# Performance work log

Measured on AMD Instinct MI355X. Metric: run time of the kernel, lower is better.

## Reference

```python
import jax, jax.numpy as jnp
import numpy as np

D_MODEL = 1024
NHEAD = 16
HEAD_DIM = D_MODEL // NHEAD
SF_THRESHOLD = 4.0
SF_LEVELS = 8
STEP = SF_THRESHOLD / SF_LEVELS  # quantization step of ScaleAndFireNeuron
EPS = 1e-6


def setup_inputs() -> dict:
    key = jax.random.key(0)
    ks = jax.random.split(key, 12)
    B, L, D = 2, 2048, D_MODEL
    s = 1.0 / np.sqrt(D)
    inp = {
        "x": jax.random.normal(ks[0], (B, L, D), dtype=jnp.float32),
        "wq": jax.random.normal(ks[1], (D, D), dtype=jnp.float32) * s,
        "bq": jnp.zeros((D,), dtype=jnp.float32),
        "wk": jax.random.normal(ks[2], (D, D), dtype=jnp.float32) * s,
        "bk": jnp.zeros((D,), dtype=jnp.float32),
        "wv": jax.random.normal(ks[3], (D, D), dtype=jnp.float32) * s,
        "bv": jnp.zeros((D,), dtype=jnp.float32),
        "wo": jax.random.normal(ks[4], (D, D), dtype=jnp.float32) * s,
        "bo": jnp.zeros((D,), dtype=jnp.float32),
        "gq": jnp.ones((HEAD_DIM,), dtype=jnp.float32),  # SpikingQKNorm gain (q)
        "gk": jnp.ones((HEAD_DIM,), dtype=jnp.float32),  # SpikingQKNorm gain (k)
    }
    return inp


def _rms_norm(t, g):
    # SpikingQKNorm: RMS normalization over head_dim with learned gain
    return t * jax.lax.rsqrt(jnp.mean(t * t, axis=-1, keepdims=True) + EPS) * g


def _sfn(t):
    # ScaleAndFireNeuron: T=1 multi-level spike quantization with straight-through estimator.
    # Levels are integer multiples of STEP, clipped to +/- SF_LEVELS.
    q = jnp.clip(jnp.round(t / STEP), -SF_LEVELS, SF_LEVELS) * STEP
    return t + jax.lax.stop_gradient(q - t)


def reference(x, wq, bq, wk, bk, wv, bv, wo, bo, gq, gk):
    B, L, D = x.shape
    H, Dh = NHEAD, HEAD_DIM
    scale = Dh ** -0.5

    def proj(w, b):
        return (x @ w.T + b).reshape(B, L, H, Dh).transpose(0, 2, 1, 3)  # [B,H,L,Dh]

    q = _sfn(_rms_norm(proj(wq, bq), gq))
    k = _sfn(_rms_norm(proj(wk, bk), gk))
    v = _sfn(proj(wv, bv))

    scores = jnp.einsum('bhqd,bhkd->bhqk', q, k) * scale  # [B,H,L,L]
    probs = jax.nn.softmax(scores, axis=-1)
    out = jnp.einsum('bhqk,bhkd->bhqd', probs, v)  # [B,H,L,Dh]
    out = out.transpose(0, 2, 1, 3).reshape(B, L, D)
    return out @ wo.T + bo
```

## Files before the change

kernel.cpp:

```cpp
#include <hip/hip_runtime.h>
#include <stdint.h>

#define D_MODEL 1024
#define NHEAD 16
#define HEAD_DIM 64
#define SEQ 2048
#define BATCH 2
#define MROWS (BATCH*SEQ)
#define KVBLK 128
#define KVTILES (SEQ/KVBLK)

typedef unsigned short u16;
typedef short bf16x8 __attribute__((ext_vector_type(8)));
typedef float f32x4 __attribute__((ext_vector_type(4)));
typedef float f32x16 __attribute__((ext_vector_type(16)));

__device__ inline float bf2f(u16 h){ return __uint_as_float(((unsigned)h)<<16); }
__device__ inline u16 f2bf(float x){
  unsigned u = __float_as_uint(x);
  unsigned r = (u + 0x7FFFu + ((u>>16)&1u)) >> 16;
  return (u16)r;
}

__device__ inline f32x4 mfma_bf16(bf16x8 a, bf16x8 b, f32x4 c){
  return __builtin_amdgcn_mfma_f32_16x16x32_bf16(a, b, c, 0, 0, 0);
}
__device__ inline f32x16 mfma32_bf16(bf16x8 a, bf16x8 b, f32x16 c){
  return __builtin_amdgcn_mfma_f32_32x32x16_bf16(a, b, c, 0, 0, 0);
}

__device__ inline void gld_lds16(const u16* g, u16* l){
  __builtin_amdgcn_global_load_lds(
      (const __attribute__((address_space(1))) void*)g,
      (__attribute__((address_space(3))) void*)l, 16, 0, 0);
}

__device__ inline int swz8(int row){ return (row ^ (row >> 3)) & 7; }

__device__ inline uint32_t pack_bf2(float p0, float p1){
  uint32_t u0 = __float_as_uint(p0) + 0x8000u;
  uint32_t u1 = __float_as_uint(p1) + 0x8000u;
  return __builtin_amdgcn_perm(u1, u0, 0x07060302u);
}

__global__ __launch_bounds__(256) void pack_all(
    const float* __restrict__ x,
    const float* __restrict__ wq, const float* __restrict__ wk,
    const float* __restrict__ wv, const float* __restrict__ wo,
    u16* __restrict__ x_hi, u16* __restrict__ x_lo,
    u16* __restrict__ qkv_hi, u16* __restrict__ qkv_lo,
    u16* __restrict__ wo_hi)
{
  int b = blockIdx.x;
  const float* src;
  u16 *hi, *lo;
  int i;
  if (b < 4096){
    src = x; i = b*256 + threadIdx.x;
    hi = x_hi; lo = x_lo;
  } else {
    int which = (b - 4096) >> 10;
    i = ((b - 4096) & 1023)*256 + threadIdx.x;
    src = which==0 ? wq : which==1 ? wk : which==2 ? wv : wo;
    if (which == 3){ hi = wo_hi; lo = nullptr; }
    else { hi = qkv_hi + ((size_t)which << 20); lo = qkv_lo + ((size_t)which << 20); }
  }
  float4 v = ((const float4*)src)[i];
  float vv[4] = {v.x, v.y, v.z, v.w};
  u16 h[4], l[4];
  #pragma unroll
  for (int j=0;j<4;j++){
    h[j] = f2bf(vv[j]);
    l[j] = f2bf(vv[j] - bf2f(h[j]));
  }
  ((ushort4*)hi)[i] = make_ushort4(h[0],h[1],h[2],h[3]);
  if (lo) ((ushort4*)lo)[i] = make_ushort4(l[0],l[1],l[2],l[3]);
}

__global__ __launch_bounds__(256) void gemm_qkv(
    const u16* __restrict__ a_hi, const u16* __restrict__ a_lo,
    const u16* __restrict__ b_hi, const u16* __restrict__ b_lo,
    const float* __restrict__ bq, const float* __restrict__ bk_,
    const float* __restrict__ bv,
    u16* __restrict__ qb, u16* __restrict__ kb, u16* __restrict__ vb,
    const float* __restrict__ gq, const float* __restrict__ gk)
{
  __shared__ u16 lds[2][12288];
  const int tid = threadIdx.x;
  const int lane = tid & 63;
  const int w = tid >> 6;
  const int wr = w >> 1, wc = w & 1;
  const int m0 = blockIdx.x * 128;
  const int n0 = blockIdx.y * 128;
  const int K = 1024;

  f32x4 acc[4][4];
  #pragma unroll
  for (int i=0;i<4;i++)
    #pragma unroll
    for (int j=0;j<4;j++) acc[i][j] = (f32x4){0.f,0.f,0.f,0.f};

  auto stage = [&](int buf, int kt){
    u16* base = &lds[buf][0];
    if (kt < 32){
      int kk = kt << 5;
      #pragma unroll
      for (int r=0;r<2;r++){
        const u16* g = a_hi + (size_t)(m0 + (tid>>2) + r*64)*K + kk + (tid&3)*8;
        gld_lds16(g, base + w*512 + r*2048);
      }
      #pragma unroll
      for (int r=0;r<2;r++){
        const u16* g = a_lo + (size_t)(m0 + (tid>>2) + r*64)*K + kk + (tid&3)*8;
        gld_lds16(g, base + 4096 + w*512 + r*2048);
      }
      #pragma unroll
      for (int r=0;r<2;r++){
        const u16* g = b_hi + (size_t)(n0 + (tid>>2) + r*64)*K + kk + (tid&3)*8;
        gld_lds16(g, base + 8192 + w*512 + r*2048);
      }
    } else {
      int kk = (kt-32) << 5;
      #pragma unroll
      for (int r=0;r<2;r++){
        const u16* g = a_hi + (size_t)(m0 + (tid>>2) + r*64)*K + kk + (tid&3)*8;
        gld_lds16(g, base + w*512 + r*2048);
      }
      #pragma unroll
      for (int r=0;r<2;r++){
        const u16* g = b_lo + (size_t)(n0 + (tid>>2) + r*64)*K + kk + (tid&3)*8;
        gld_lds16(g, base + 8192 + w*512 + r*2048);
      }
    }
  };

  const int koff = (lane>>4)*8;
  const int rowa = wr*64 + (lane&15);
  const int rowb = wc*64 + (lane&15);

  stage(0, 0);
  for (int kt=0; kt<64; ++kt){
    __syncthreads();
    if (kt+1 < 64) stage((kt+1)&1, kt+1);
    const u16* la = &lds[kt&1][0];
    const u16* lb = &lds[kt&1][8192];
    bf16x8 bfv[4];
    #pragma unroll
    for (int j=0;j<4;j++) bfv[j] = *(const bf16x8*)&lb[(rowb + j*16)*32 + koff];
    bf16x8 af[4];
    #pragma unroll
    for (int i=0;i<4;i++) af[i] = *(const bf16x8*)&la[(rowa + i*16)*32 + koff];
    #pragma unroll
    for (int i=0;i<4;i++)
      #pragma unroll
      for (int j=0;j<4;j++)
        acc[i][j] = mfma_bf16(af[i], bfv[j], acc[i][j]);
    if (kt < 32){
      const u16* ll = &lds[kt&1][4096];
      bf16x8 al[4];
      #pragma unroll
      for (int i=0;i<4;i++) al[i] = *(const bf16x8*)&ll[(rowa + i*16)*32 + koff];
      #pragma unroll
      for (int i=0;i<4;i++)
        #pragma unroll
        for (int j=0;j<4;j++)
          acc[i][j] = mfma_bf16(al[i], bfv[j], acc[i][j]);
    }
  }

  const int gcolbase = n0 + wc*64;
  const int sidx = gcolbase >> 6;
  const int ttype = sidx < 16 ? 0 : (sidx < 32 ? 1 : 2);
  u16* dst = ttype==0 ? qb : (ttype==1 ? kb : vb);
  const float* bsrc = ttype==0 ? bq : (ttype==1 ? bk_ : bv);
  const int h = sidx - (ttype==1 ? 16 : (ttype==2 ? 32 : 0));
  float gvals[4], bvals[4];
  #pragma unroll
  for (int j=0;j<4;j++){
    int dh = j*16 + (lane&15);
    bvals[j] = bsrc[((gcolbase & 1023) + dh) & 1023];
    gvals[j] = ttype==0 ? gq[dh] : (ttype==1 ? gk[dh] : 1.0f);
  }
  #pragma unroll
  for (int i=0;i<4;i++){
    #pragma unroll
    for (int r=0;r<4;r++){
      float tv[4];
      float ssq = 0.f;
      #pragma unroll
      for (int j=0;j<4;j++){ tv[j] = acc[i][j][r] + bvals[j]; ssq += tv[j]*tv[j]; }
      ssq += __shfl_xor(ssq, 1);
      ssq += __shfl_xor(ssq, 2);
      ssq += __shfl_xor(ssq, 4);
      ssq += __shfl_xor(ssq, 8);
      float s = 1.0f;
      if (ttype < 2) s = 1.0f / sqrtf(ssq * (1.0f/64.0f) + 1e-6f);
      int row = m0 + wr*64 + i*16 + (lane>>4)*4 + r;
      int bi = row >> 11, li = row & 2047;
      size_t obase = ((size_t)(bi*NHEAD + h)*SEQ + li)*HEAD_DIM;
      #pragma unroll
      for (int j=0;j<4;j++){
        float val = tv[j] * s * gvals[j];
        float z = rintf(val * 2.0f);
        z = fminf(8.0f, fmaxf(-8.0f, z));
        dst[obase + j*16 + (lane&15)] = f2bf(z * 0.5f);
      }
    }
  }
}

__global__ __launch_bounds__(256) void gemm_bt(
    const u16* __restrict__ a_hi, const u16* __restrict__ b_hi,
    const float* __restrict__ bias, float* __restrict__ out_f,
    int M, int N, int K)
{
  __shared__ u16 lds[2][8192];
  const int tid = threadIdx.x;
  const int lane = tid & 63;
  const int w = tid >> 6;
  const int wr = w >> 1, wc = w & 1;
  const int m0 = blockIdx.x * 128;
  const int n0 = blockIdx.y * 128;
  const int NT = K / 32;

  f32x4 acc[4][4];
  #pragma unroll
  for (int i=0;i<4;i++)
    #pragma unroll
    for (int j=0;j<4;j++) acc[i][j] = (f32x4){0.f,0.f,0.f,0.f};

  auto stage = [&](int buf, int kt){
    int kk = kt * 32;
    u16* base = &lds[buf][0];
    #pragma unroll
    for (int r=0;r<2;r++){
      const u16* g = a_hi + (size_t)(m0 + (tid>>2) + r*64)*K + kk + (tid&3)*8;
      gld_lds16(g, base + w*512 + r*2048);
    }
    #pragma unroll
    for (int r=0;r<2;r++){
      const u16* g = b_hi + (size_t)(n0 + (tid>>2) + r*64)*K + kk + (tid&3)*8;
      gld_lds16(g, base + 4096 + w*512 + r*2048);
    }
  };

  stage(0, 0);
  for (int kt=0; kt<NT; ++kt){
    __syncthreads();
    if (kt+1 < NT) stage((kt+1)&1, kt+1);
    const u16* la = &lds[kt&1][0];
    const u16* lb = &lds[kt&1][4096];
    const int koff = (lane>>4)*8;
    const int rowa = wr*64 + (lane&15);
    const int rowb = wc*64 + (lane&15);
    bf16x8 af[4], bfv[4];
    #pragma unroll
    for (int i=0;i<4;i++) af[i]  = *(const bf16x8*)&la[(rowa + i*16)*32 + koff];
    #pragma unroll
    for (int i=0;i<4;i++) bfv[i] = *(const bf16x8*)&lb[(rowb + i*16)*32 + koff];
    #pragma unroll
    for (int i=0;i<4;i++)
      #pragma unroll
      for (int j=0;j<4;j++)
        acc[i][j] = mfma_bf16(af[i], bfv[j], acc[i][j]);
  }

  const int gcolbase = n0 + wc*64;
  #pragma unroll
  for (int j=0;j<4;j++){
    float bj = bias[gcolbase + j*16 + (lane&15)];
    #pragma unroll
    for (int i=0;i<4;i++){
      int row = m0 + wr*64 + i*16 + (lane>>4)*4;
      #pragma unroll
      for (int r=0;r<4;r++)
        out_f[(size_t)(row+r)*N + gcolbase + j*16 + (lane&15)] = acc[i][j][r] + bj;
    }
  }
}

__global__ __launch_bounds__(256) void transpose_v(const u16* __restrict__ v, u16* __restrict__ vt){
  __shared__ u16 tl[64][66];
  int bh = blockIdx.x >> 5;
  int l0 = (blockIdx.x & 31) * 64;
  int tid = threadIdx.x;
  #pragma unroll
  for (int it=0; it<2; ++it){
    int idx = tid + it*256;
    int row = idx >> 3, g = idx & 7;
    bf16x8 d = *(const bf16x8*)(v + ((size_t)bh*SEQ + l0 + row)*64 + g*8);
    #pragma unroll
    for (int j=0;j<8;j++) tl[row][g*8+j] = (u16)d[j];
  }
  __syncthreads();
  #pragma unroll
  for (int it=0; it<2; ++it){
    int idx = tid + it*256;
    int dh = idx >> 3, g = idx & 7;
    u16 tmp[8];
    #pragma unroll
    for (int j=0;j<8;j++) tmp[j] = tl[g*8+j][dh];
    *(bf16x8*)(vt + ((size_t)bh*HEAD_DIM + dh)*SEQ + l0 + g*8) = *(const bf16x8*)tmp;
  }
}

__global__ __launch_bounds__(256) void attn_kernel(
    const u16* __restrict__ qb, const u16* __restrict__ kb, const u16* __restrict__ vt,
    u16* __restrict__ attn_out)
{
  __shared__ u16 lds_k[2][KVBLK*64];
  __shared__ u16 lds_v[2][64*KVBLK];
  const int tid = threadIdx.x, lane = tid & 63, w = tid >> 6;
  const int bh = blockIdx.y;
  const int q0 = blockIdx.x * 128;
  const size_t kvbase = (size_t)bh * SEQ * HEAD_DIM;
  const size_t vtbase = (size_t)bh * HEAD_DIM * SEQ;
  const int l31 = lane & 31, hi = lane >> 5;

  bf16x8 qf[4];
  #pragma unroll
  for (int kd=0; kd<4; kd++){
    const u16* g = qb + kvbase + (size_t)(q0 + w*32 + l31)*64 + kd*16 + hi*8;
    bf16x8 v = *(const bf16x8*)g;
    #pragma unroll
    for (int j=0;j<8;j++) ((u16*)&v)[j] = f2bf(bf2f((u16)v[j]) * 0.125f);
    qf[kd] = v;
  }

  float l_s = 0.f;
  f32x16 o0, o1;
  #pragma unroll
  for (int r=0;r<16;r++){ o0[r] = 0.f; o1[r] = 0.f; }

  auto stage = [&](int buf, int t){
    const int kv0 = t * KVBLK;
    #pragma unroll
    for (int r=0;r<4;r++){
      int idx = tid + r*256;
      int row = idx >> 3, grp = idx & 7;
      const u16* g = kb + kvbase + (size_t)(kv0 + row)*64 + ((grp ^ swz8(row))<<3);
      gld_lds16(g, &lds_k[buf][idx<<3]);
    }
    #pragma unroll
    for (int r=0;r<4;r++){
      int idx = tid + r*256;
      int row = idx >> 4, grp = idx & 15;
      const u16* g = vt + vtbase + (size_t)row*SEQ + kv0 + ((grp ^ swz8(row))<<3);
      gld_lds16(g, &lds_v[buf][idx<<3]);
    }
  };

  stage(0, 0);
  for (int t=0; t<KVTILES; ++t){
    __syncthreads();
    if (t+1 < KVTILES) stage((t+1)&1, t+1);
    const int buf = t & 1;

    #pragma unroll
    for (int half=0; half<2; ++half){
      f32x16 s0, s1;
      #pragma unroll
      for (int r=0;r<16;r++){ s0[r] = 0.f; s1[r] = 0.f; }
      const int row0 = half*64 + l31;
      const int row1 = half*64 + 32 + l31;
      __builtin_amdgcn_s_setprio(1);
      #pragma unroll
      for (int kd=0; kd<4; kd++){
        bf16x8 a0 = *(const bf16x8*)&lds_k[buf][row0*64 + (((kd*2+hi) ^ swz8(row0))<<3)];
        bf16x8 a1 = *(const bf16x8*)&lds_k[buf][row1*64 + (((kd*2+hi) ^ swz8(row1))<<3)];
        s0 = mfma32_bf16(a0, qf[kd], s0);
        s1 = mfma32_bf16(a1, qf[kd], s1);
      }
      __builtin_amdgcn_s_setprio(0);

      float rsum = 0.f;
      #pragma unroll
      for (int r=0;r<16;r++){ float p = __expf(s0[r]); s0[r] = p; rsum += p; }
      #pragma unroll
      for (int r=0;r<16;r++){ float p = __expf(s1[r]); s1[r] = p; rsum += p; }
      rsum += __shfl_xor(rsum, 32);
      l_s += rsum;

      uint32_t W[2][4][2];
      #pragma unroll
      for (int g=0; g<4; g++){
        W[0][g][0] = pack_bf2(s0[g*4+0], s0[g*4+1]);
        W[0][g][1] = pack_bf2(s0[g*4+2], s0[g*4+3]);
        W[1][g][0] = pack_bf2(s1[g*4+0], s1[g*4+1]);
        W[1][g][1] = pack_bf2(s1[g*4+2], s1[g*4+3]);
      }
      bf16x8 pa[4];
      #pragma unroll
      for (int ks=0; ks<4; ks++){
        const int kvb = ks >> 1, ks0 = ks & 1;
        uint32_t own0 = hi ? W[kvb][ks0*2+1][0] : W[kvb][ks0*2][0];
        uint32_t own1 = hi ? W[kvb][ks0*2+1][1] : W[kvb][ks0*2][1];
        uint32_t t0   = hi ? W[kvb][ks0*2][0]   : W[kvb][ks0*2+1][0];
        uint32_t t1   = hi ? W[kvb][ks0*2][1]   : W[kvb][ks0*2+1][1];
        uint32_t sw0  = (uint32_t)__shfl_xor((int)t0, 32);
        uint32_t sw1  = (uint32_t)__shfl_xor((int)t1, 32);
        uint32_t words[4];
        words[0] = hi ? sw0 : own0;
        words[1] = hi ? sw1 : own1;
        words[2] = hi ? own0 : sw0;
        words[3] = hi ? own1 : sw1;
        pa[ks] = *(const bf16x8*)words;
      }

      __builtin_amdgcn_s_setprio(1);
      #pragma unroll
      for (int ks=0; ks<4; ks++){
        const int rv0 = l31, rv1 = 32 + l31;
        const int cg = half*8 + ks*2 + hi;
        bf16x8 vb0 = *(const bf16x8*)&lds_v[buf][rv0*KVBLK + ((cg ^ swz8(rv0))<<3)];
        bf16x8 vb1 = *(const bf16x8*)&lds_v[buf][rv1*KVBLK + ((cg ^ swz8(rv1))<<3)];
        o0 = mfma32_bf16(pa[ks], vb0, o0);
        o1 = mfma32_bf16(pa[ks], vb1, o1);
      }
      __builtin_amdgcn_s_setprio(0);
    }
  }

  const int b = bh >> 4, h = bh & 15;
  #pragma unroll
  for (int r=0;r<16;r++){
    int q = (r&3) + 8*(r>>2) + 4*hi;
    float linv = 1.0f / __shfl(l_s, q);
    int row = q0 + w*32 + q;
    size_t obase = ((size_t)b*SEQ + row)*D_MODEL + h*64;
    attn_out[obase + l31]      = f2bf(o0[r] * linv);
    attn_out[obase + 32 + l31] = f2bf(o1[r] * linv);
  }
}

extern "C" void kernel_launch(void* const* d_in, const int* in_sizes, int n_in,
                              void* d_out, int out_size, void* d_ws, size_t ws_size,
                              hipStream_t stream){
  const float* x  = (const float*)d_in[0];
  const float* wq = (const float*)d_in[1];
  const float* bq = (const float*)d_in[2];
  const float* wk = (const float*)d_in[3];
  const float* bk = (const float*)d_in[4];
  const float* wv = (const float*)d_in[5];
  const float* bv = (const float*)d_in[6];
  const float* wo = (const float*)d_in[7];
  const float* bo = (const float*)d_in[8];
  const float* gq = (const float*)d_in[9];
  const float* gk = (const float*)d_in[10];
  float* out = (float*)d_out;

  char* ws = (char*)d_ws;
  size_t off = 0;
  auto alloc = [&](size_t bytes) -> char* {
    char* p = ws + off; off += (bytes + 255) & ~(size_t)255; return p;
  };
  const size_t ND = (size_t)MROWS * D_MODEL;
  u16* x_hi    = (u16*)alloc(ND*2);
  u16* x_lo    = (u16*)alloc(ND*2);
  u16* wqkv_hi = (u16*)alloc((size_t)3072*1024*2);
  u16* wqkv_lo = (u16*)alloc((size_t)3072*1024*2);
  u16* wo_hi   = (u16*)alloc((size_t)1024*1024*2);
  u16* q_bf    = (u16*)alloc(ND*2);
  u16* k_bf    = (u16*)alloc(ND*2);
  u16* v_bf    = (u16*)alloc(ND*2);
  u16* vT      = (u16*)alloc(ND*2);
  u16* attn_bf = (u16*)alloc(ND*2);
  (void)ws_size; (void)in_sizes; (void)n_in; (void)out_size;

  pack_all<<<8192, 256, 0, stream>>>(x, wq, wk, wv, wo,
        x_hi, x_lo, wqkv_hi, wqkv_lo, wo_hi);

  gemm_qkv<<<dim3(32,24), 256, 0, stream>>>(x_hi, x_lo, wqkv_hi, wqkv_lo,
        bq, bk, bv, q_bf, k_bf, v_bf, gq, gk);

  transpose_v<<<1024, 256, 0, stream>>>(v_bf, vT);

  attn_kernel<<<dim3(16,32), 256, 0, stream>>>(q_bf, k_bf, vT, attn_bf);

  gemm_bt<<<dim3(32,8), 256, 0, stream>>>(attn_bf, wo_hi, bo, out, MROWS, 1024, 1024);
}
```

Baseline: 172.8 us.

## Switch GEMMs to fp16 split precision and write V transposed from QKV epilogue

Moves the hi/lo split packing and the projection GEMMs from bf16 to fp16 MFMA, and stores the attention output in fp16. This gives more mantissa bits per term and may allow a cheaper split later. Separately, the QKV GEMM epilogue now writes V directly in transposed layout with ushort4 stores, which removes the transpose_v kernel launch and its round trip through memory. fp16 can overflow if activations grow large, and the transposed stores are strided along SEQ, so they may coalesce less well.

New measurement: 170.9 us. About the same (-1.1%).

```diff
diff --git a/kernel.cpp b/kernel.cpp
--- a/kernel.cpp
+++ b/kernel.cpp
@@ -12,6 +12,7 @@
 
 typedef unsigned short u16;
 typedef short bf16x8 __attribute__((ext_vector_type(8)));
+typedef _Float16 f16x8 __attribute__((ext_vector_type(8)));
 typedef float f32x4 __attribute__((ext_vector_type(4)));
 typedef float f32x16 __attribute__((ext_vector_type(16)));
 
@@ -21,9 +22,11 @@
   unsigned r = (u + 0x7FFFu + ((u>>16)&1u)) >> 16;
   return (u16)r;
 }
-
-__device__ inline f32x4 mfma_bf16(bf16x8 a, bf16x8 b, f32x4 c){
-  return __builtin_amdgcn_mfma_f32_16x16x32_bf16(a, b, c, 0, 0, 0);
+__device__ inline u16 f2h(float x){ _Float16 h = (_Float16)x; return *(u16*)&h; }
+__device__ inline float h2f(u16 b){ _Float16 h = *(_Float16*)&b; return (float)h; }
+
+__device__ inline f32x4 mfma_f16(f16x8 a, f16x8 b, f32x4 c){
+  return __builtin_amdgcn_mfma_f32_16x16x32_f16(a, b, c, 0, 0, 0);
 }
 __device__ inline f32x16 mfma32_bf16(bf16x8 a, bf16x8 b, f32x16 c){
   return __builtin_amdgcn_mfma_f32_32x32x16_bf16(a, b, c, 0, 0, 0);
@@ -48,41 +51,49 @@
     const float* __restrict__ wq, const float* __restrict__ wk,
     const float* __restrict__ wv, const float* __restrict__ wo,
     u16* __restrict__ x_hi, u16* __restrict__ x_lo,
-    u16* __restrict__ qkv_hi, u16* __restrict__ qkv_lo,
-    u16* __restrict__ wo_hi)
+    u16* __restrict__ qkv_h, u16* __restrict__ qkv_lo,
+    u16* __restrict__ wo_h)
 {
   int b = blockIdx.x;
-  const float* src;
-  u16 *hi, *lo;
-  int i;
   if (b < 4096){
-    src = x; i = b*256 + threadIdx.x;
-    hi = x_hi; lo = x_lo;
+    int i = b*256 + threadIdx.x;
+    float4 v = ((const float4*)x)[i];
+    float vv[4] = {v.x, v.y, v.z, v.w};
+    u16 h[4], l[4];
+    #pragma unroll
+    for (int j=0;j<4;j++){
+      h[j] = f2h(vv[j]);
+      l[j] = f2h(vv[j] - h2f(h[j]));
+    }
+    ((ushort4*)x_hi)[i] = make_ushort4(h[0],h[1],h[2],h[3]);
+    ((ushort4*)x_lo)[i] = make_ushort4(l[0],l[1],l[2],l[3]);
   } else {
     int which = (b - 4096) >> 10;
-    i = ((b - 4096) & 1023)*256 + threadIdx.x;
-    src = which==0 ? wq : which==1 ? wk : which==2 ? wv : wo;
-    if (which == 3){ hi = wo_hi; lo = nullptr; }
-    else { hi = qkv_hi + ((size_t)which << 20); lo = qkv_lo + ((size_t)which << 20); }
-  }
-  float4 v = ((const float4*)src)[i];
-  float vv[4] = {v.x, v.y, v.z, v.w};
-  u16 h[4], l[4];
-  #pragma unroll
-  for (int j=0;j<4;j++){
-    h[j] = f2bf(vv[j]);
-    l[j] = f2bf(vv[j] - bf2f(h[j]));
-  }
-  ((ushort4*)hi)[i] = make_ushort4(h[0],h[1],h[2],h[3]);
-  if (lo) ((ushort4*)lo)[i] = make_ushort4(l[0],l[1],l[2],l[3]);
+    int i = ((b - 4096) & 1023)*256 + threadIdx.x;
+    const float* src = which==0 ? wq : which==1 ? wk : which==2 ? wv : wo;
+    float4 v = ((const float4*)src)[i];
+    float vv[4] = {v.x, v.y, v.z, v.w};
+    u16 h[4];
+    #pragma unroll
+    for (int j=0;j<4;j++) h[j] = f2h(vv[j]);
+    if (which == 3){
+      ((ushort4*)wo_h)[i] = make_ushort4(h[0],h[1],h[2],h[3]);
+    } else {
+      u16 l[4];
+      #pragma unroll
+      for (int j=0;j<4;j++) l[j] = f2h(vv[j] - h2f(h[j]));
+      ((ushort4*)(qkv_h  + ((size_t)which << 20)))[i] = make_ushort4(h[0],h[1],h[2],h[3]);
+      ((ushort4*)(qkv_lo + ((size_t)which << 20)))[i] = make_ushort4(l[0],l[1],l[2],l[3]);
+    }
+  }
 }
 
 __global__ __launch_bounds__(256) void gemm_qkv(
     const u16* __restrict__ a_hi, const u16* __restrict__ a_lo,
-    const u16* __restrict__ b_hi, const u16* __restrict__ b_lo,
+    const u16* __restrict__ b_h,  const u16* __restrict__ b_lo,
     const float* __restrict__ bq, const float* __restrict__ bk_,
     const float* __restrict__ bv,
-    u16* __restrict__ qb, u16* __restrict__ kb, u16* __restrict__ vb,
+    u16* __restrict__ qb, u16* __restrict__ kb, u16* __restrict__ vt,
     const float* __restrict__ gq, const float* __restrict__ gk)
 {
   __shared__ u16 lds[2][12288];
@@ -90,6 +101,7 @@
   const int lane = tid & 63;
   const int w = tid >> 6;
   const int wr = w >> 1, wc = w & 1;
+  const int l15 = lane & 15, lq = lane >> 4;
   const int m0 = blockIdx.x * 128;
   const int n0 = blockIdx.y * 128;
   const int K = 1024;
@@ -116,7 +128,7 @@
       }
       #pragma unroll
       for (int r=0;r<2;r++){
-        const u16* g = b_hi + (size_t)(n0 + (tid>>2) + r*64)*K + kk + (tid&3)*8;
+        const u16* g = b_h + (size_t)(n0 + (tid>>2) + r*64)*K + kk + (tid&3)*8;
         gld_lds16(g, base + 8192 + w*512 + r*2048);
       }
     } else {
@@ -134,9 +146,9 @@
     }
   };
 
-  const int koff = (lane>>4)*8;
-  const int rowa = wr*64 + (lane&15);
-  const int rowb = wc*64 + (lane&15);
+  const int koff = lq*8;
+  const int rowa = wr*64 + l15;
+  const int rowb = wc*64 + l15;
 
   stage(0, 0);
   for (int kt=0; kt<64; ++kt){
@@ -144,73 +156,99 @@
     if (kt+1 < 64) stage((kt+1)&1, kt+1);
     const u16* la = &lds[kt&1][0];
     const u16* lb = &lds[kt&1][8192];
-    bf16x8 bfv[4];
-    #pragma unroll
-    for (int j=0;j<4;j++) bfv[j] = *(const bf16x8*)&lb[(rowb + j*16)*32 + koff];
-    bf16x8 af[4];
-    #pragma unroll
-    for (int i=0;i<4;i++) af[i] = *(const bf16x8*)&la[(rowa + i*16)*32 + koff];
+    f16x8 bfv[4];
+    #pragma unroll
+    for (int j=0;j<4;j++) bfv[j] = *(const f16x8*)&lb[(rowb + j*16)*32 + koff];
+    f16x8 af[4];
+    #pragma unroll
+    for (int i=0;i<4;i++) af[i] = *(const f16x8*)&la[(rowa + i*16)*32 + koff];
     #pragma unroll
     for (int i=0;i<4;i++)
       #pragma unroll
       for (int j=0;j<4;j++)
-        acc[i][j] = mfma_bf16(af[i], bfv[j], acc[i][j]);
+        acc[i][j] = mfma_f16(af[i], bfv[j], acc[i][j]);
     if (kt < 32){
       const u16* ll = &lds[kt&1][4096];
-      bf16x8 al[4];
-      #pragma unroll
-      for (int i=0;i<4;i++) al[i] = *(const bf16x8*)&ll[(rowa + i*16)*32 + koff];
+      f16x8 al[4];
+      #pragma unroll
+      for (int i=0;i<4;i++) al[i] = *(const f16x8*)&ll[(rowa + i*16)*32 + koff];
       #pragma unroll
       for (int i=0;i<4;i++)
         #pragma unroll
         for (int j=0;j<4;j++)
-          acc[i][j] = mfma_bf16(al[i], bfv[j], acc[i][j]);
+          acc[i][j] = mfma_f16(al[i], bfv[j], acc[i][j]);
     }
   }
 
   const int gcolbase = n0 + wc*64;
   const int sidx = gcolbase >> 6;
   const int ttype = sidx < 16 ? 0 : (sidx < 32 ? 1 : 2);
-  u16* dst = ttype==0 ? qb : (ttype==1 ? kb : vb);
-  const float* bsrc = ttype==0 ? bq : (ttype==1 ? bk_ : bv);
-  const int h = sidx - (ttype==1 ? 16 : (ttype==2 ? 32 : 0));
-  float gvals[4], bvals[4];
-  #pragma unroll
-  for (int j=0;j<4;j++){
-    int dh = j*16 + (lane&15);
-    bvals[j] = bsrc[((gcolbase & 1023) + dh) & 1023];
-    gvals[j] = ttype==0 ? gq[dh] : (ttype==1 ? gk[dh] : 1.0f);
-  }
-  #pragma unroll
-  for (int i=0;i<4;i++){
-    #pragma unroll
-    for (int r=0;r<4;r++){
-      float tv[4];
-      float ssq = 0.f;
-      #pragma unroll
-      for (int j=0;j<4;j++){ tv[j] = acc[i][j][r] + bvals[j]; ssq += tv[j]*tv[j]; }
-      ssq += __shfl_xor(ssq, 1);
-      ssq += __shfl_xor(ssq, 2);
-      ssq += __shfl_xor(ssq, 4);
-      ssq += __shfl_xor(ssq, 8);
-      float s = 1.0f;
-      if (ttype < 2) s = 1.0f / sqrtf(ssq * (1.0f/64.0f) + 1e-6f);
-      int row = m0 + wr*64 + i*16 + (lane>>4)*4 + r;
-      int bi = row >> 11, li = row & 2047;
-      size_t obase = ((size_t)(bi*NHEAD + h)*SEQ + li)*HEAD_DIM;
+
+  if (ttype < 2){
+    u16* dst = ttype==0 ? qb : kb;
+    const float* bsrc = ttype==0 ? bq : bk_;
+    const int h = sidx - (ttype==1 ? 16 : 0);
+    float gvals[4], bvals[4];
+    #pragma unroll
+    for (int j=0;j<4;j++){
+      int dh = j*16 + l15;
+      bvals[j] = bsrc[(gcolbase & 1023) + dh];
+      gvals[j] = ttype==0 ? gq[dh] : gk[dh];
+    }
+    #pragma unroll
+    for (int i=0;i<4;i++){
+      #pragma unroll
+      for (int r=0;r<4;r++){
+        float tv[4];
+        float ssq = 0.f;
+        #pragma unroll
+        for (int j=0;j<4;j++){ tv[j] = acc[i][j][r] + bvals[j]; ssq += tv[j]*tv[j]; }
+        ssq += __shfl_xor(ssq, 1);
+        ssq += __shfl_xor(ssq, 2);
+        ssq += __shfl_xor(ssq, 4);
+        ssq += __shfl_xor(ssq, 8);
+        float s = 1.0f / sqrtf(ssq * (1.0f/64.0f) + 1e-6f);
+        int row = m0 + wr*64 + i*16 + lq*4 + r;
+        int bi = row >> 11, li = row & 2047;
+        size_t obase = ((size_t)(bi*NHEAD + h)*SEQ + li)*HEAD_DIM;
+        #pragma unroll
+        for (int j=0;j<4;j++){
+          float val = tv[j] * s * gvals[j];
+          float z = rintf(val * 2.0f);
+          z = fminf(8.0f, fmaxf(-8.0f, z));
+          dst[obase + j*16 + l15] = f2bf(z * 0.5f);
+        }
+      }
+    }
+  } else {
+    const int h = sidx - 32;
+    float bvals[4];
+    #pragma unroll
+    for (int j=0;j<4;j++) bvals[j] = bv[(gcolbase - 2048) + j*16 + l15];
+    #pragma unroll
+    for (int i=0;i<4;i++){
+      int row0 = m0 + wr*64 + i*16 + lq*4;
+      int bi = row0 >> 11, li0 = row0 & 2047;
       #pragma unroll
       for (int j=0;j<4;j++){
-        float val = tv[j] * s * gvals[j];
-        float z = rintf(val * 2.0f);
-        z = fminf(8.0f, fmaxf(-8.0f, z));
-        dst[obase + j*16 + (lane&15)] = f2bf(z * 0.5f);
+        u16 h4[4];
+        #pragma unroll
+        for (int r=0;r<4;r++){
+          float val = acc[i][j][r] + bvals[j];
+          float z = rintf(val * 2.0f);
+          z = fminf(8.0f, fmaxf(-8.0f, z));
+          h4[r] = f2bf(z * 0.5f);
+        }
+        int dh = j*16 + l15;
+        *(ushort4*)&vt[(((size_t)(bi*NHEAD + h))*HEAD_DIM + dh)*SEQ + li0] =
+            make_ushort4(h4[0],h4[1],h4[2],h4[3]);
       }
     }
   }
 }
 
 __global__ __launch_bounds__(256) void gemm_bt(
-    const u16* __restrict__ a_hi, const u16* __restrict__ b_hi,
+    const u16* __restrict__ a_h, const u16* __restrict__ b_h,
     const float* __restrict__ bias, float* __restrict__ out_f,
     int M, int N, int K)
 {
@@ -234,12 +272,12 @@
     u16* base = &lds[buf][0];
     #pragma unroll
     for (int r=0;r<2;r++){
-      const u16* g = a_hi + (size_t)(m0 + (tid>>2) + r*64)*K + kk + (tid&3)*8;
+      const u16* g = a_h + (size_t)(m0 + (tid>>2) + r*64)*K + kk + (tid&3)*8;
       gld_lds16(g, base + w*512 + r*2048);
     }
     #pragma unroll
     for (int r=0;r<2;r++){
-      const u16* g = b_hi + (size_t)(n0 + (tid>>2) + r*64)*K + kk + (tid&3)*8;
+      const u16* g = b_h + (size_t)(n0 + (tid>>2) + r*64)*K + kk + (tid&3)*8;
       gld_lds16(g, base + 4096 + w*512 + r*2048);
     }
   };
@@ -253,16 +291,16 @@
     const int koff = (lane>>4)*8;
     const int rowa = wr*64 + (lane&15);
     const int rowb = wc*64 + (lane&15);
-    bf16x8 af[4], bfv[4];
-    #pragma unroll
-    for (int i=0;i<4;i++) af[i]  = *(const bf16x8*)&la[(rowa + i*16)*32 + koff];
-    #pragma unroll
-    for (int i=0;i<4;i++) bfv[i] = *(const bf16x8*)&lb[(rowb + i*16)*32 + koff];
+    f16x8 af[4], bfv[4];
+    #pragma unroll
+    for (int i=0;i<4;i++) af[i]  = *(const f16x8*)&la[(rowa + i*16)*32 + koff];
+    #pragma unroll
+    for (int i=0;i<4;i++) bfv[i] = *(const f16x8*)&lb[(rowb + i*16)*32 + koff];
     #pragma unroll
     for (int i=0;i<4;i++)
       #pragma unroll
       for (int j=0;j<4;j++)
-        acc[i][j] = mfma_bf16(af[i], bfv[j], acc[i][j]);
+        acc[i][j] = mfma_f16(af[i], bfv[j], acc[i][j]);
   }
 
   const int gcolbase = n0 + wc*64;
@@ -276,31 +314,6 @@
       for (int r=0;r<4;r++)
         out_f[(size_t)(row+r)*N + gcolbase + j*16 + (lane&15)] = acc[i][j][r] + bj;
     }
-  }
-}
-
-__global__ __launch_bounds__(256) void transpose_v(const u16* __restrict__ v, u16* __restrict__ vt){
-  __shared__ u16 tl[64][66];
-  int bh = blockIdx.x >> 5;
-  int l0 = (blockIdx.x & 31) * 64;
-  int tid = threadIdx.x;
-  #pragma unroll
-  for (int it=0; it<2; ++it){
-    int idx = tid + it*256;
-    int row = idx >> 3, g = idx & 7;
-    bf16x8 d = *(const bf16x8*)(v + ((size_t)bh*SEQ + l0 + row)*64 + g*8);
-    #pragma unroll
-    for (int j=0;j<8;j++) tl[row][g*8+j] = (u16)d[j];
-  }
-  __syncthreads();
-  #pragma unroll
-  for (int it=0; it<2; ++it){
-    int idx = tid + it*256;
-    int dh = idx >> 3, g = idx & 7;
-    u16 tmp[8];
-    #pragma unroll
-    for (int j=0;j<8;j++) tmp[j] = tl[g*8+j][dh];
-    *(bf16x8*)(vt + ((size_t)bh*HEAD_DIM + dh)*SEQ + l0 + g*8) = *(const bf16x8*)tmp;
   }
 }
 
@@ -428,8 +441,8 @@
     float linv = 1.0f / __shfl(l_s, q);
     int row = q0 + w*32 + q;
     size_t obase = ((size_t)b*SEQ + row)*D_MODEL + h*64;
-    attn_out[obase + l31]      = f2bf(o0[r] * linv);
-    attn_out[obase + 32 + l31] = f2bf(o1[r] * linv);
+    attn_out[obase + l31]      = f2h(o0[r] * linv);
+    attn_out[obase + 32 + l31] = f2h(o1[r] * linv);
   }
 }
 
@@ -457,25 +470,22 @@
   const size_t ND = (size_t)MROWS * D_MODEL;
   u16* x_hi    = (u16*)alloc(ND*2);
   u16* x_lo    = (u16*)alloc(ND*2);
-  u16* wqkv_hi = (u16*)alloc((size_t)3072*1024*2);
+  u16* wqkv_h  = (u16*)alloc((size_t)3072*1024*2);
   u16* wqkv_lo = (u16*)alloc((size_t)3072*1024*2);
-  u16* wo_hi   = (u16*)alloc((size_t)1024*1024*2);
+  u16* wo_h    = (u16*)alloc((size_t)1024*1024*2);
   u16* q_bf    = (u16*)alloc(ND*2);
   u16* k_bf    = (u16*)alloc(ND*2);
-  u16* v_bf    = (u16*)alloc(ND*2);
   u16* vT      = (u16*)alloc(ND*2);
-  u16* attn_bf = (u16*)alloc(ND*2);
+  u16* attn_h  = (u16*)alloc(ND*2);
   (void)ws_size; (void)in_sizes; (void)n_in; (void)out_size;
 
   pack_all<<<8192, 256, 0, stream>>>(x, wq, wk, wv, wo,
-        x_hi, x_lo, wqkv_hi, wqkv_lo, wo_hi);
-
-  gemm_qkv<<<dim3(32,24), 256, 0, stream>>>(x_hi, x_lo, wqkv_hi, wqkv_lo,
-        bq, bk, bv, q_bf, k_bf, v_bf, gq, gk);
-
-  transpose_v<<<1024, 256, 0, stream>>>(v_bf, vT);
-
-  attn_kernel<<<dim3(16,32), 256, 0, stream>>>(q_bf, k_bf, vT, attn_bf);
-
-  gemm_bt<<<dim3(32,8), 256, 0, stream>>>(attn_bf, wo_hi, bo, out, MROWS, 1024, 1024);
-}
+        x_hi, x_lo, wqkv_h, wqkv_lo, wo_h);
+
+  gemm_qkv<<<dim3(32,24), 256, 0, stream>>>(x_hi, x_lo, wqkv_h, wqkv_lo,
+        bq, bk, bv, q_bf, k_bf, vT, gq, gk);
+
+  attn_kernel<<<dim3(16,32), 256, 0, stream>>>(q_bf, k_bf, vT, attn_h);
+
+  gemm_bt<<<dim3(32,8), 256, 0, stream>>>(attn_h, wo_h, bo, out, MROWS, 1024, 1024);
+}
```
